# Optimization experiments

Measured on AMD Instinct MI355X. Metric: run time of the kernel, lower is better.

The kernel has to match this reference:

```python
import jax, jax.numpy as jnp
import numpy as np

D = 448  # state_dim == input_dim == output_dim

def _param(key, shape):
    # matches torch.rand(shape) * 0.1 + 0.001
    return jax.random.uniform(key, shape, dtype=jnp.float32) * 0.1 + 0.001

def setup_inputs() -> dict:
    key = jax.random.key(0)
    ks = jax.random.split(key, 9)
    x = jax.random.normal(ks[0], (8, 4096, D), dtype=jnp.float32)
    return {
        "x": x,
        "W_q": _param(ks[1], (D, D)),
        "W_k": _param(ks[2], (D, D)),
        "W_v": _param(ks[3], (D, D)),
        "W_o": _param(ks[4], (D, D)),
        "SSM_A": _param(ks[5], (D, D)),
        "SSM_B": _param(ks[6], (D, D)),
        "SSM_C": _param(ks[7], (D, D)),
    }

def reference(x, W_q, W_k, W_v, W_o, SSM_A, SSM_B, SSM_C):
    # seq_len=4096 > threshold=256 -> quadratic SSM path.
    # structured_processing's einsum 'bsd,dd->bsd' multiplies elementwise by
    # the diagonal of the matrix; the block loop is redundant, so we apply the
    # diagonal scale over the whole sequence in one fused op.
    q = jnp.einsum('bsi,id->bsd', x, W_q)
    k = jnp.einsum('bsi,id->bsd', x, W_k)
    v = jnp.einsum('bsi,id->bsd', x, W_v)
    ssm = (q * jnp.diagonal(SSM_A)
           + k * jnp.diagonal(SSM_B)
           + v * jnp.diagonal(SSM_C))
    # dropout is identity in eval mode
    return jnp.einsum('bsd,do->bso', ssm, W_o)
```

## Files before the change

kernel.cpp:

```cpp
#include <hip/hip_runtime.h>
#include <hip/hip_bf16.h>

#define DDIM 448
#define NSTEP 14

typedef __hip_bfloat16 bf16;
typedef __attribute__((ext_vector_type(8))) short short8;
typedef __attribute__((ext_vector_type(4))) float f32x4;

__device__ __forceinline__ short bf_bits(float f) {
    bf16 h = __float2bfloat16(f);
    return *reinterpret_cast<short*>(&h);
}

__device__ __forceinline__ void async16(const bf16* g, bf16* l) {
    __builtin_amdgcn_global_load_lds(
        (const __attribute__((address_space(1))) void*)g,
        (__attribute__((address_space(3))) void*)l, 16, 0, 0);
}

__global__ __launch_bounds__(256) void prep_wc(
    const float* __restrict__ Wq, const float* __restrict__ Wk,
    const float* __restrict__ Wv, const float* __restrict__ Wo,
    const float* __restrict__ Ad, const float* __restrict__ Bd,
    const float* __restrict__ Cd, bf16* __restrict__ Wt)
{
    __shared__ __align__(16) bf16 As[64 * 32];
    __shared__ __align__(16) bf16 Bs[64 * 32];
    __shared__ float da[DDIM], db[DDIM], dc[DDIM];

    const int tid  = threadIdx.x;
    const int i0   = blockIdx.x * 64;
    const int o0   = blockIdx.y * 64;
    const int lane = tid & 63;
    const int wid  = tid >> 6;
    const int wm   = wid >> 1, wn = wid & 1;
    const int m_   = lane & 15, kq = lane >> 4;

    for (int d = tid; d < DDIM; d += 256) {
        da[d] = Ad[d * DDIM + d];
        db[d] = Bd[d * DDIM + d];
        dc[d] = Cd[d * DDIM + d];
    }

    const int dr  = tid >> 3;
    const int oc8 = (tid & 7) * 8;
    const int ir  = tid >> 2;
    const int dc8 = (tid & 3) * 8;

    f32x4 acc[2][2] = {};

    f32x4 w0 = *(const f32x4*)(Wo + dr * DDIM + o0 + oc8);
    f32x4 w1 = *(const f32x4*)(Wo + dr * DDIM + o0 + oc8 + 4);
    f32x4 q0 = *(const f32x4*)(Wq + (i0 + ir) * DDIM + dc8);
    f32x4 q1 = *(const f32x4*)(Wq + (i0 + ir) * DDIM + dc8 + 4);
    f32x4 t0 = *(const f32x4*)(Wk + (i0 + ir) * DDIM + dc8);
    f32x4 t1 = *(const f32x4*)(Wk + (i0 + ir) * DDIM + dc8 + 4);
    f32x4 v0 = *(const f32x4*)(Wv + (i0 + ir) * DDIM + dc8);
    f32x4 v1 = *(const f32x4*)(Wv + (i0 + ir) * DDIM + dc8 + 4);

    for (int k0 = 0; k0 < DDIM; k0 += 32) {
        __syncthreads();
        #pragma unroll
        for (int j = 0; j < 4; ++j) {
            As[(oc8 + j) * 32 + dr]     = __float2bfloat16(w0[j]);
            As[(oc8 + 4 + j) * 32 + dr] = __float2bfloat16(w1[j]);
        }
        short8 e;
        #pragma unroll
        for (int j = 0; j < 4; ++j) {
            e[j]     = bf_bits(q0[j] * da[k0 + dc8 + j]
                             + t0[j] * db[k0 + dc8 + j]
                             + v0[j] * dc[k0 + dc8 + j]);
            e[j + 4] = bf_bits(q1[j] * da[k0 + dc8 + 4 + j]
                             + t1[j] * db[k0 + dc8 + 4 + j]
                             + v1[j] * dc[k0 + dc8 + 4 + j]);
        }
        *(short8*)&Bs[ir * 32 + dc8] = e;
        __syncthreads();

        const int kn = (k0 + 32 < DDIM) ? k0 + 32 : 0;
        w0 = *(const f32x4*)(Wo + (kn + dr) * DDIM + o0 + oc8);
        w1 = *(const f32x4*)(Wo + (kn + dr) * DDIM + o0 + oc8 + 4);
        q0 = *(const f32x4*)(Wq + (i0 + ir) * DDIM + kn + dc8);
        q1 = *(const f32x4*)(Wq + (i0 + ir) * DDIM + kn + dc8 + 4);
        t0 = *(const f32x4*)(Wk + (i0 + ir) * DDIM + kn + dc8);
        t1 = *(const f32x4*)(Wk + (i0 + ir) * DDIM + kn + dc8 + 4);
        v0 = *(const f32x4*)(Wv + (i0 + ir) * DDIM + kn + dc8);
        v1 = *(const f32x4*)(Wv + (i0 + ir) * DDIM + kn + dc8 + 4);

        short8 af[2], bfr[2];
        #pragma unroll
        for (int mi = 0; mi < 2; ++mi)
            af[mi] = *(const short8*)&As[(wm * 32 + mi * 16 + m_) * 32 + kq * 8];
        #pragma unroll
        for (int ni = 0; ni < 2; ++ni)
            bfr[ni] = *(const short8*)&Bs[(wn * 32 + ni * 16 + m_) * 32 + kq * 8];
        #pragma unroll
        for (int mi = 0; mi < 2; ++mi)
            #pragma unroll
            for (int ni = 0; ni < 2; ++ni)
                acc[mi][ni] = __builtin_amdgcn_mfma_f32_16x16x32_bf16(
                    af[mi], bfr[ni], acc[mi][ni], 0, 0, 0);
    }

    #pragma unroll
    for (int mi = 0; mi < 2; ++mi)
        #pragma unroll
        for (int ni = 0; ni < 2; ++ni) {
            const int o = o0 + wm * 32 + mi * 16 + kq * 4;
            const int i = i0 + wn * 32 + ni * 16 + m_;
            bf16* dst = Wt + (i >> 5) * (DDIM * 32) + (i & 31);
            #pragma unroll
            for (int r = 0; r < 4; ++r)
                dst[(o + r) * 32] = __float2bfloat16(acc[mi][ni][r]);
        }
}

__global__ __launch_bounds__(512, 2) void gemm_xwc(
    const float* __restrict__ X, const bf16* __restrict__ Wt,
    float* __restrict__ out)
{
    __shared__ __align__(16) char smem[102400];

    const int tid  = threadIdx.x;
    const int lane = tid & 63;
    const int wid  = tid >> 6;
    const int wr   = wid >> 2;
    const int wc   = wid & 3;
    const int m_   = lane & 15;
    const int kq   = lane >> 4;
    const int row0 = blockIdx.x * 128;

    const int ar  = tid >> 2;
    const int ac4 = tid & 3;
    const float* agp = X + (row0 + ar) * DDIM + ac4 * 8;

    const int lsw = (lane * 16) ^ (((lane >> 3) & 7) << 4);
    const bf16* bgp = Wt + wc * 7 * 512 + (lsw >> 1);
    const int fb  = m_ * 64 + kq * 16;
    const int fsw = fb ^ (((fb >> 7) & 7) << 4);
    const int ab  = ar * 64 + ac4 * 16;
    const int asw = ab ^ (((ab >> 7) & 7) << 4);

    f32x4 acc[4][7] = {};

    f32x4 a0 = *(const f32x4*)(agp);
    f32x4 a1 = *(const f32x4*)(agp + 4);
    {
        short8 w;
        #pragma unroll
        for (int j = 0; j < 4; ++j) {
            w[j] = bf_bits(a0[j]); w[j + 4] = bf_bits(a1[j]);
        }
        *(short8*)(smem + asw) = w;
    }
    a0 = *(const f32x4*)(agp + 32);
    a1 = *(const f32x4*)(agp + 36);
    if (wid < 4) {
        bf16* B0 = (bf16*)(smem + 16384);
        bf16* B1 = (bf16*)(smem + 16384 + 28672);
        #pragma unroll
        for (int j = 0; j < 7; ++j)
            async16(bgp + j * 512, B0 + (wc * 7 + j) * 512);
        const bf16* b1 = bgp + DDIM * 32;
        #pragma unroll
        for (int j = 0; j < 7; ++j)
            async16(b1 + j * 512, B1 + (wc * 7 + j) * 512);
    }
    asm volatile("s_waitcnt vmcnt(7)" ::: "memory");
    asm volatile("s_waitcnt lgkmcnt(0)" ::: "memory");
    __builtin_amdgcn_s_barrier();

    int bcur = 0;
    int bn2  = 2;
    for (int s = 0; s < NSTEP; ++s) {
        const char* AcB = (const char*)smem + ((s & 1) << 13) + wr * 4096;
        const char* BcB = (const char*)smem + 16384 + bcur * 28672 + wc * 7168;

        if (s + 1 < NSTEP) {
            char* An = (char*)smem + (((s + 1) & 1) << 13);
            short8 w;
            #pragma unroll
            for (int j = 0; j < 4; ++j) {
                w[j] = bf_bits(a0[j]); w[j + 4] = bf_bits(a1[j]);
            }
            *(short8*)(An + asw) = w;
        }
        if (s + 2 < NSTEP) {
            const int k2 = (s + 2) * 32;
            a0 = *(const f32x4*)(agp + k2);
            a1 = *(const f32x4*)(agp + k2 + 4);
        }
        if (s + 2 < NSTEP && wid < 4) {
            bf16* Bn = (bf16*)(smem + 16384 + bn2 * 28672);
            const bf16* bsrc = bgp + (s + 2) * (DDIM * 32);
            #pragma unroll
            for (int j = 0; j < 7; ++j)
                async16(bsrc + j * 512, Bn + (wc * 7 + j) * 512);
        }

        short8 af[4], bfr[7];
        #pragma unroll
        for (int mi = 0; mi < 4; ++mi)
            af[mi] = *(const short8*)(AcB + mi * 1024 + fsw);
        #pragma unroll
        for (int ni = 0; ni < 7; ++ni)
            bfr[ni] = *(const short8*)(BcB + ni * 1024 + fsw);

        #pragma unroll
        for (int mi = 0; mi < 4; ++mi)
            #pragma unroll
            for (int ni = 0; ni < 7; ++ni)
                acc[mi][ni] = __builtin_amdgcn_mfma_f32_16x16x32_bf16(
                    af[mi], bfr[ni], acc[mi][ni], 0, 0, 0);

        if (s < NSTEP - 2) {
            asm volatile("s_waitcnt vmcnt(9)" ::: "memory");
        } else {
            asm volatile("s_waitcnt vmcnt(0)" ::: "memory");
        }
        asm volatile("s_waitcnt lgkmcnt(0)" ::: "memory");
        __builtin_amdgcn_s_barrier();

        bcur = (bcur == 2) ? 0 : bcur + 1;
        bn2  = (bn2  == 2) ? 0 : bn2  + 1;
    }

    {
        const int crow = row0 + wr * 64 + kq * 4;
        const int ccol = wc * 112 + m_;
        #pragma unroll
        for (int mi = 0; mi < 4; ++mi)
            #pragma unroll
            for (int ni = 0; ni < 7; ++ni) {
                float* dst = out + (crow + mi * 16) * DDIM + ccol + ni * 16;
                #pragma unroll
                for (int r = 0; r < 4; ++r)
                    dst[r * DDIM] = acc[mi][ni][r];
            }
    }
}

extern "C" void kernel_launch(void* const* d_in, const int* in_sizes, int n_in,
                              void* d_out, int out_size, void* d_ws, size_t ws_size,
                              hipStream_t stream) {
    const float* x  = (const float*)d_in[0];
    const float* Wq = (const float*)d_in[1];
    const float* Wk = (const float*)d_in[2];
    const float* Wv = (const float*)d_in[3];
    const float* Wo = (const float*)d_in[4];
    const float* Ad = (const float*)d_in[5];
    const float* Bd = (const float*)d_in[6];
    const float* Cd = (const float*)d_in[7];

    bf16*  Wt  = (bf16*)d_ws;
    float* out = (float*)d_out;

    const int M = in_sizes[0] / DDIM;

    prep_wc<<<dim3(7, 7), 256, 0, stream>>>(Wq, Wk, Wv, Wo, Ad, Bd, Cd, Wt);
    gemm_xwc<<<M / 128, 512, 0, stream>>>(x, Wt, out);
}
```

Baseline: 140.1 us.

## Double K tile to 64 per stage with two-buffer pipeline and all-wave B loads

Restructures the main GEMM loop to process K=64 per barrier step (7 steps instead of 14), using double-buffered A and B tiles instead of a triple-buffered B ring. All 8 waves now issue the async B loads rather than only 4, and the loop is fully unrolled. It also drops the XOR swizzle on LDS addresses, which halves the barrier count and spreads the load issue across waves. In exchange, LDS grows to 144KB, which likely drops occupancy from 2 blocks to 1 per CU, and it risks LDS bank conflicts and a shallower prefetch distance for B.

```diff
diff --git a/kernel.cpp b/kernel.cpp
--- a/kernel.cpp
+++ b/kernel.cpp
@@ -2,7 +2,7 @@
 #include <hip/hip_bf16.h>
 
 #define DDIM 448
-#define NSTEP 14
+#define NS2 7
 
 typedef __hip_bfloat16 bf16;
 typedef __attribute__((ext_vector_type(8))) short short8;
@@ -121,7 +121,7 @@
     const float* __restrict__ X, const bf16* __restrict__ Wt,
     float* __restrict__ out)
 {
-    __shared__ __align__(16) char smem[102400];
+    __shared__ __align__(16) char smem[147456];
 
     const int tid  = threadIdx.x;
     const int lane = tid & 63;
@@ -132,99 +132,104 @@
     const int kq   = lane >> 4;
     const int row0 = blockIdx.x * 128;
 
-    const int ar  = tid >> 2;
-    const int ac4 = tid & 3;
-    const float* agp = X + (row0 + ar) * DDIM + ac4 * 8;
-
-    const int lsw = (lane * 16) ^ (((lane >> 3) & 7) << 4);
-    const bf16* bgp = Wt + wc * 7 * 512 + (lsw >> 1);
-    const int fb  = m_ * 64 + kq * 16;
-    const int fsw = fb ^ (((fb >> 7) & 7) << 4);
-    const int ab  = ar * 64 + ac4 * 16;
-    const int asw = ab ^ (((ab >> 7) & 7) << 4);
+    const int arow = (tid >> 1) & 127;
+    const int acol = (tid >> 8) * 32 + (tid & 1) * 16;
+    const float* agp = X + (row0 + arow) * DDIM + acol;
+    const int awb = tid * 32;
+
+    const bf16* bgp = Wt + wid * 3584 + lane * 8;
 
     f32x4 acc[4][7] = {};
-
-    f32x4 a0 = *(const f32x4*)(agp);
-    f32x4 a1 = *(const f32x4*)(agp + 4);
+    f32x4 a0, a1, a2, a3;
+
+    a0 = *(const f32x4*)(agp);
+    a1 = *(const f32x4*)(agp + 4);
+    a2 = *(const f32x4*)(agp + 8);
+    a3 = *(const f32x4*)(agp + 12);
     {
-        short8 w;
+        char* A0 = (char*)smem;
+        short8 w0, w1;
         #pragma unroll
         for (int j = 0; j < 4; ++j) {
-            w[j] = bf_bits(a0[j]); w[j + 4] = bf_bits(a1[j]);
-        }
-        *(short8*)(smem + asw) = w;
-    }
-    a0 = *(const f32x4*)(agp + 32);
-    a1 = *(const f32x4*)(agp + 36);
-    if (wid < 4) {
-        bf16* B0 = (bf16*)(smem + 16384);
-        bf16* B1 = (bf16*)(smem + 16384 + 28672);
+            w0[j] = bf_bits(a0[j]); w0[j + 4] = bf_bits(a1[j]);
+            w1[j] = bf_bits(a2[j]); w1[j + 4] = bf_bits(a3[j]);
+        }
+        *(short8*)(A0 + awb)      = w0;
+        *(short8*)(A0 + awb + 16) = w1;
+    }
+    {
+        bf16* B0 = (bf16*)(smem + 32768);
         #pragma unroll
         for (int j = 0; j < 7; ++j)
-            async16(bgp + j * 512, B0 + (wc * 7 + j) * 512);
-        const bf16* b1 = bgp + DDIM * 32;
-        #pragma unroll
-        for (int j = 0; j < 7; ++j)
-            async16(b1 + j * 512, B1 + (wc * 7 + j) * 512);
-    }
-    asm volatile("s_waitcnt vmcnt(7)" ::: "memory");
+            async16(bgp + j * 512, B0 + wid * 3584 + j * 512);
+    }
+    asm volatile("" ::: "memory");
+    a0 = *(const f32x4*)(agp + 64);
+    a1 = *(const f32x4*)(agp + 68);
+    a2 = *(const f32x4*)(agp + 72);
+    a3 = *(const f32x4*)(agp + 76);
+    asm volatile("s_waitcnt vmcnt(4)" ::: "memory");
     asm volatile("s_waitcnt lgkmcnt(0)" ::: "memory");
     __builtin_amdgcn_s_barrier();
 
-    int bcur = 0;
-    int bn2  = 2;
-    for (int s = 0; s < NSTEP; ++s) {
-        const char* AcB = (const char*)smem + ((s & 1) << 13) + wr * 4096;
-        const char* BcB = (const char*)smem + 16384 + bcur * 28672 + wc * 7168;
-
-        if (s + 1 < NSTEP) {
-            char* An = (char*)smem + (((s + 1) & 1) << 13);
-            short8 w;
+    #pragma unroll
+    for (int s = 0; s < NS2; ++s) {
+        const char* AcB = (const char*)smem + (s & 1) * 16384 + wr * 4096;
+        const char* BcB = (const char*)smem + 32768 + (s & 1) * 57344 + wc * 7168;
+
+        if (s + 1 < NS2) {
+            bf16* Bn = (bf16*)(smem + 32768 + ((s + 1) & 1) * 57344);
+            const bf16* bsrc = bgp + (s + 1) * 28672;
+            #pragma unroll
+            for (int j = 0; j < 7; ++j)
+                async16(bsrc + j * 512, Bn + wid * 3584 + j * 512);
+        }
+        asm volatile("" ::: "memory");
+        if (s + 1 < NS2) {
+            char* An = (char*)smem + (((s + 1) & 1)) * 16384;
+            short8 w0, w1;
             #pragma unroll
             for (int j = 0; j < 4; ++j) {
-                w[j] = bf_bits(a0[j]); w[j + 4] = bf_bits(a1[j]);
+                w0[j] = bf_bits(a0[j]); w0[j + 4] = bf_bits(a1[j]);
+                w1[j] = bf_bits(a2[j]); w1[j + 4] = bf_bits(a3[j]);
             }
-            *(short8*)(An + asw) = w;
-        }
-        if (s + 2 < NSTEP) {
-            const int k2 = (s + 2) * 32;
+            *(short8*)(An + awb)      = w0;
+            *(short8*)(An + awb + 16) = w1;
+        }
+        if (s + 2 < NS2) {
+            const int k2 = (s + 2) * 64;
             a0 = *(const f32x4*)(agp + k2);
             a1 = *(const f32x4*)(agp + k2 + 4);
-        }
-        if (s + 2 < NSTEP && wid < 4) {
-            bf16* Bn = (bf16*)(smem + 16384 + bn2 * 28672);
-            const bf16* bsrc = bgp + (s + 2) * (DDIM * 32);
-            #pragma unroll
-            for (int j = 0; j < 7; ++j)
-                async16(bsrc + j * 512, Bn + (wc * 7 + j) * 512);
-        }
-
-        short8 af[4], bfr[7];
-        #pragma unroll
-        for (int mi = 0; mi < 4; ++mi)
-            af[mi] = *(const short8*)(AcB + mi * 1024 + fsw);
-        #pragma unroll
-        for (int ni = 0; ni < 7; ++ni)
-            bfr[ni] = *(const short8*)(BcB + ni * 1024 + fsw);
-
-        #pragma unroll
-        for (int mi = 0; mi < 4; ++mi)
+            a2 = *(const f32x4*)(agp + k2 + 8);
+            a3 = *(const f32x4*)(agp + k2 + 12);
+        }
+
+        #pragma unroll
+        for (int g = 0; g < 2; ++g) {
+            short8 af[4], bfr[7];
+            #pragma unroll
+            for (int mi = 0; mi < 4; ++mi)
+                af[mi] = *(const short8*)(AcB + g * 8192 + mi * 1024
+                                          + m_ * 64 + kq * 16);
             #pragma unroll
             for (int ni = 0; ni < 7; ++ni)
-                acc[mi][ni] = __builtin_amdgcn_mfma_f32_16x16x32_bf16(
-                    af[mi], bfr[ni], acc[mi][ni], 0, 0, 0);
-
-        if (s < NSTEP - 2) {
-            asm volatile("s_waitcnt vmcnt(9)" ::: "memory");
+                bfr[ni] = *(const short8*)(BcB + g * 28672 + ni * 1024
+                                           + m_ * 64 + kq * 16);
+            #pragma unroll
+            for (int mi = 0; mi < 4; ++mi)
+                #pragma unroll
+                for (int ni = 0; ni < 7; ++ni)
+                    acc[mi][ni] = __builtin_amdgcn_mfma_f32_16x16x32_bf16(
+                        af[mi], bfr[ni], acc[mi][ni], 0, 0, 0);
+        }
+
+        if (s + 2 < NS2) {
+            asm volatile("s_waitcnt vmcnt(4)" ::: "memory");
         } else {
             asm volatile("s_waitcnt vmcnt(0)" ::: "memory");
         }
         asm volatile("s_waitcnt lgkmcnt(0)" ::: "memory");
         __builtin_amdgcn_s_barrier();
-
-        bcur = (bcur == 2) ? 0 : bcur + 1;
-        bn2  = (bn2  == 2) ? 0 : bn2  + 1;
     }
 
     {
```

Result: no change. 142.1 us (+1.4%).
